# Performance work log

Measured on AMD Instinct MI355X. Metric: run time of the kernel, lower is better.

The kernel has to match this reference:

```python
import jax, jax.numpy as jnp
import numpy as np

# gaussian_radial_function width: gamma = 1/(2*sigma^2), sigma = radii spacing (2/7)
GAMMA = 6.125


def setup_inputs() -> dict:
    key = jax.random.key(0)
    k1, k2, k3, k4, k5 = jax.random.split(key, 5)
    n, b, a, c, d, r = 4, 256, 256, 16, 16, 8
    inp = jax.random.normal(k1, (n, c, a), dtype=jnp.float32)
    difference_mat = jax.random.normal(k2, (n, b, a, 3), dtype=jnp.float32)
    relative_mask = jax.random.uniform(k3, (n, b, a), dtype=jnp.float32)
    W = jax.random.normal(k4, (d, c, r), dtype=jnp.float32) / np.float32(np.sqrt(c * r))
    radii = jax.random.uniform(k5, (r,), dtype=jnp.float32) * 2.0
    return {"input": inp, "difference_mat": difference_mat,
            "relative_mask": relative_mask, "W": W, "radii": radii}


def reference(input, difference_mat, relative_mask, W, radii):
    # distances |x_b - x_a|: [n, b, a]
    dist = jnp.sqrt(jnp.sum(difference_mat * difference_mat, axis=-1))
    # gaussian radial basis: [n, b, a, r]
    R = jnp.exp(-GAMMA * (dist[..., None] - radii) ** 2)
    # apply relative mask (kernel = mask[n,b,a] * kernel[d,c,n,b,a] in original)
    R = R * relative_mask[..., None]
    # kernel[d,c,n,b,a] = sum_r W[d,c,r] * R[n,b,a,r]; fused with the
    # contraction 'nca,dcnba->ndb' into a single einsum.
    return jnp.einsum('nca,dcr,nbar->ndb', input, W, R)
```

## Files before the change

### kernel.cpp

```cpp
#include <hip/hip_runtime.h>
#include <math.h>

constexpr int N = 4, B = 256, A = 256, C = 16, D = 16, RR = 8;
constexpr int DR = D * RR;
constexpr int BT = 4;
constexpr float GAMMA = 6.125f;

__global__ __launch_bounds__(256) void se3_compute_P(
    const float* __restrict__ input, const float* __restrict__ W,
    float* __restrict__ P)
{
    const int blk = blockIdx.x;
    const int n  = blk >> 7;
    const int a2 = blk & 127;
    const int al = threadIdx.x >> 7;
    const int dr = threadIdx.x & 127;
    const int a  = a2 * 2 + al;
    const int d  = dr >> 3;
    const int r  = dr & 7;

    float s = 0.f;
#pragma unroll
    for (int c = 0; c < C; ++c) {
        s += W[(d * C + c) * RR + r] * input[(n * C + c) * A + a];
    }
    P[((size_t)(n * A) + a) * DR + dr] = s;
}

__global__ __launch_bounds__(512) void se3_compute_out(
    const float* __restrict__ P, const float* __restrict__ diff,
    const float* __restrict__ mask, const float* __restrict__ radii,
    float* __restrict__ out)
{
    const int blk = blockIdx.x;
    const int n  = blk / (B / BT);
    const int b0 = (blk % (B / BT)) * BT;
    const int h  = threadIdx.x >> 8;
    const int a  = threadIdx.x & 255;
    const int lane = threadIdx.x & 63;
    const int wave = threadIdx.x >> 6;

    float rad[RR];
#pragma unroll
    for (int r = 0; r < RR; ++r) rad[r] = radii[r];

    float preg[DR / 2];
    const float* Pt = P + ((size_t)(n * A) + a) * DR + h * (DR / 2);
#pragma unroll
    for (int j = 0; j < DR / 2; ++j) preg[j] = Pt[j];

    __shared__ float lds[BT][8][8];

#pragma unroll
    for (int bi = 0; bi < BT; ++bi) {
        const int b = b0 + bi;
        const size_t nba = (size_t)(n * B + b) * A + a;
        const float* dp = diff + nba * 3;
        const float dx = dp[0], dy = dp[1], dz = dp[2];
        const float dist = sqrtf(dx * dx + dy * dy + dz * dz);
        const float m = mask[nba];

        float R[RR];
#pragma unroll
        for (int r = 0; r < RR; ++r) {
            const float t = dist - rad[r];
            R[r] = m * __expf(-GAMMA * t * t);
        }

        float acc[8];
#pragma unroll
        for (int dl = 0; dl < 8; ++dl) {
            float s = 0.f;
#pragma unroll
            for (int r = 0; r < RR; ++r) s += R[r] * preg[dl * RR + r];
            acc[dl] = s;
        }

        {
            const bool hi = (lane & 32) != 0;
#pragma unroll
            for (int i = 0; i < 4; ++i) {
                float send = hi ? acc[i] : acc[i + 4];
                float recv = __shfl_xor(send, 32, 64);
                acc[i] = (hi ? acc[i + 4] : acc[i]) + recv;
            }
        }
        {
            const bool hi = (lane & 16) != 0;
#pragma unroll
            for (int i = 0; i < 2; ++i) {
                float send = hi ? acc[i] : acc[i + 2];
                float recv = __shfl_xor(send, 16, 64);
                acc[i] = (hi ? acc[i + 2] : acc[i]) + recv;
            }
        }
        {
            const bool hi = (lane & 8) != 0;
            float send = hi ? acc[0] : acc[1];
            float recv = __shfl_xor(send, 8, 64);
            acc[0] = (hi ? acc[1] : acc[0]) + recv;
        }
        float v = acc[0];
        v += __shfl_xor(v, 1, 64);
        v += __shfl_xor(v, 2, 64);
        v += __shfl_xor(v, 4, 64);
        if ((lane & 7) == 0) lds[bi][wave][(lane >> 3) & 7] = v;
    }
    __syncthreads();

    if (threadIdx.x < BT * D) {
        const int bi = threadIdx.x >> 4;
        const int d  = threadIdx.x & 15;
        const int hh = d >> 3;
        const int dl = d & 7;
        const float s = lds[bi][hh * 4 + 0][dl] + lds[bi][hh * 4 + 1][dl]
                      + lds[bi][hh * 4 + 2][dl] + lds[bi][hh * 4 + 3][dl];
        out[(n * D + d) * B + (b0 + bi)] = s;
    }
}

__global__ __launch_bounds__(256) void se3_fused(
    const float* __restrict__ input, const float* __restrict__ diff,
    const float* __restrict__ mask, const float* __restrict__ W,
    const float* __restrict__ radii, float* __restrict__ out)
{
    const int blk = blockIdx.x;
    const int n = blk / B;
    const int b = blk % B;
    const int a = threadIdx.x;

    __shared__ float Wl[D * C * RR];
    for (int i = threadIdx.x; i < D * C * RR; i += 256) Wl[i] = W[i];
    __syncthreads();

    const size_t nba = (size_t)(n * B + b) * A + a;
    const float* dp = diff + nba * 3;
    const float dx = dp[0], dy = dp[1], dz = dp[2];
    const float dist = sqrtf(dx * dx + dy * dy + dz * dz);
    const float m = mask[nba];

    float R[RR];
#pragma unroll
    for (int r = 0; r < RR; ++r) {
        const float t = dist - radii[r];
        R[r] = m * __expf(-GAMMA * t * t);
    }

    float acc[D];
#pragma unroll
    for (int d = 0; d < D; ++d) acc[d] = 0.f;
    for (int c = 0; c < C; ++c) {
        const float x = input[(n * C + c) * A + a];
        float xr[RR];
#pragma unroll
        for (int r = 0; r < RR; ++r) xr[r] = x * R[r];
#pragma unroll
        for (int d = 0; d < D; ++d) {
#pragma unroll
            for (int r = 0; r < RR; ++r)
                acc[d] += Wl[(d * C + c) * RR + r] * xr[r];
        }
    }

    __shared__ float lds2[4 * D];
    const int lane = threadIdx.x & 63;
    const int wave = threadIdx.x >> 6;
#pragma unroll
    for (int d = 0; d < D; ++d) {
        float v = acc[d];
#pragma unroll
        for (int off = 32; off > 0; off >>= 1)
            v += __shfl_down(v, off, 64);
        if (lane == 0) lds2[wave * D + d] = v;
    }
    __syncthreads();
    if (threadIdx.x < D) {
        const int d = threadIdx.x;
        const float s = lds2[d] + lds2[D + d] + lds2[2 * D + d] + lds2[3 * D + d];
        out[(n * D + d) * B + b] = s;
    }
}

extern "C" void kernel_launch(void* const* d_in, const int* in_sizes, int n_in,
                              void* d_out, int out_size, void* d_ws, size_t ws_size,
                              hipStream_t stream) {
    const float* input = (const float*)d_in[0];
    const float* diff  = (const float*)d_in[1];
    const float* mask  = (const float*)d_in[2];
    const float* W     = (const float*)d_in[3];
    const float* radii = (const float*)d_in[4];
    float* out = (float*)d_out;

    const size_t needP = (size_t)N * A * DR * sizeof(float);
    if (ws_size >= needP) {
        float* P = (float*)d_ws;
        se3_compute_P<<<N * (A / 2), 256, 0, stream>>>(input, W, P);
        se3_compute_out<<<N * (B / BT), 512, 0, stream>>>(P, diff, mask, radii, out);
    } else {
        se3_fused<<<N * B, 256, 0, stream>>>(input, diff, mask, W, radii, out);
    }
}
```

Baseline: 17.61 us.

## Store P in float4-interleaved layout for coalesced loads in output kernel

```diff
diff --git a/kernel.cpp b/kernel.cpp
--- a/kernel.cpp
+++ b/kernel.cpp
@@ -3,32 +3,36 @@
 
 constexpr int N = 4, B = 256, A = 256, C = 16, D = 16, RR = 8;
 constexpr int DR = D * RR;
+constexpr int DR4 = DR / 4;
 constexpr int BT = 4;
 constexpr float GAMMA = 6.125f;
 
 __global__ __launch_bounds__(256) void se3_compute_P(
     const float* __restrict__ input, const float* __restrict__ W,
-    float* __restrict__ P)
+    float4* __restrict__ P4)
 {
     const int blk = blockIdx.x;
-    const int n  = blk >> 7;
-    const int a2 = blk & 127;
-    const int al = threadIdx.x >> 7;
-    const int dr = threadIdx.x & 127;
-    const int a  = a2 * 2 + al;
-    const int d  = dr >> 3;
-    const int r  = dr & 7;
-
-    float s = 0.f;
+    const int n   = blk >> 5;
+    const int dr4 = blk & 31;
+    const int d   = dr4 >> 1;
+    const int rb  = (dr4 & 1) * 4;
+    const int a   = threadIdx.x;
+
+    float acc0 = 0.f, acc1 = 0.f, acc2 = 0.f, acc3 = 0.f;
 #pragma unroll
     for (int c = 0; c < C; ++c) {
-        s += W[(d * C + c) * RR + r] * input[(n * C + c) * A + a];
-    }
-    P[((size_t)(n * A) + a) * DR + dr] = s;
+        const float x = input[(n * C + c) * A + a];
+        const float* Wdc = W + (d * C + c) * RR + rb;
+        acc0 += Wdc[0] * x;
+        acc1 += Wdc[1] * x;
+        acc2 += Wdc[2] * x;
+        acc3 += Wdc[3] * x;
+    }
+    P4[(size_t)blk * A + a] = make_float4(acc0, acc1, acc2, acc3);
 }
 
 __global__ __launch_bounds__(512) void se3_compute_out(
-    const float* __restrict__ P, const float* __restrict__ diff,
+    const float4* __restrict__ P4, const float* __restrict__ diff,
     const float* __restrict__ mask, const float* __restrict__ radii,
     float* __restrict__ out)
 {
@@ -45,9 +49,15 @@
     for (int r = 0; r < RR; ++r) rad[r] = radii[r];
 
     float preg[DR / 2];
-    const float* Pt = P + ((size_t)(n * A) + a) * DR + h * (DR / 2);
-#pragma unroll
-    for (int j = 0; j < DR / 2; ++j) preg[j] = Pt[j];
+    const float4* Pt = P4 + ((size_t)(n * DR4) + h * 16) * A + a;
+#pragma unroll
+    for (int j = 0; j < 16; ++j) {
+        const float4 v = Pt[(size_t)j * A];
+        preg[j * 4 + 0] = v.x;
+        preg[j * 4 + 1] = v.y;
+        preg[j * 4 + 2] = v.z;
+        preg[j * 4 + 3] = v.w;
+    }
 
     __shared__ float lds[BT][8][8];
 
@@ -191,11 +201,11 @@
     const float* radii = (const float*)d_in[4];
     float* out = (float*)d_out;
 
-    const size_t needP = (size_t)N * A * DR * sizeof(float);
+    const size_t needP = (size_t)N * DR * A * sizeof(float);
     if (ws_size >= needP) {
-        float* P = (float*)d_ws;
-        se3_compute_P<<<N * (A / 2), 256, 0, stream>>>(input, W, P);
-        se3_compute_out<<<N * (B / BT), 512, 0, stream>>>(P, diff, mask, radii, out);
+        float4* P4 = (float4*)d_ws;
+        se3_compute_P<<<N * DR4, 256, 0, stream>>>(input, W, P4);
+        se3_compute_out<<<N * (B / BT), 512, 0, stream>>>(P4, diff, mask, radii, out);
     } else {
         se3_fused<<<N * B, 256, 0, stream>>>(input, diff, mask, W, radii, out);
     }
```

New measurement: 14.98 us. 1.18x faster.
